# Kernel optimization log

Measured on AMD Instinct MI355X. Metric: run time of the kernel, lower is better.

Reference implementation:

```python
import jax, jax.numpy as jnp
import numpy as np

B, H, S, D = 2, 16, 2048, 64

def setup_inputs() -> dict:
    key = jax.random.key(0)
    kq, kk, kv = jax.random.split(key, 3)
    q = jax.random.normal(kq, (B, H, S, D), dtype=jnp.float32)
    k = jax.random.normal(kk, (B, H, S, D), dtype=jnp.float32)
    v = jax.random.normal(kv, (B, H, S, D), dtype=jnp.float32)
    # causal mask, broadcastable over batch and heads
    mask = jnp.tril(jnp.ones((S, S), dtype=bool))[None, None, :, :]
    return {"q": q, "k": k, "v": v, "mask": mask}

def reference(q, k, v, mask):
    d_k = q.shape[-1]
    # scores: [B, H, S, S]
    scores = jnp.einsum('bhqd,bhkd->bhqk', q, k) / (d_k ** 0.5)
    scores = jnp.where(mask, scores, -jnp.inf)
    probs = jax.nn.softmax(scores, axis=-1)  # numerically stable (max-subtracted)
    return jnp.einsum('bhqk,bhkd->bhqd', probs, v)
```

## Files before the change

### kernel.cpp

```cpp
#include <hip/hip_runtime.h>

#define S_LEN 2048
#define DHEAD 64
#define NBH   32
#define QTILE 64
#define KVTILE 64
#define NQ 32
#define LDK 72

typedef float          f32x4  __attribute__((ext_vector_type(4)));
typedef unsigned short u16x8  __attribute__((ext_vector_type(8)));
typedef unsigned int   u32x2  __attribute__((ext_vector_type(2)));
typedef unsigned int   u32x4  __attribute__((ext_vector_type(4)));
typedef __bf16         bf16x8 __attribute__((ext_vector_type(8)));

__device__ __forceinline__ unsigned int pack_bf16(float lo, float hi) {
  return __builtin_amdgcn_perm(__builtin_bit_cast(unsigned int, hi),
                               __builtin_bit_cast(unsigned int, lo),
                               0x07060302u);
}

#define KVSTRIDE 9216
#define VOFF 4608
#define PB0 18432

__global__ __launch_bounds__(256, 2)
void attn_fwd_kernel(const float* __restrict__ qg, const float* __restrict__ kg,
                     const float* __restrict__ vg, float* __restrict__ og)
{
  __shared__ unsigned short smem[23040];

  const int tid  = threadIdx.x;
  const int wid  = tid >> 6;
  const int lane = tid & 63;
  const int lr   = lane & 15;
  const int lg   = lane >> 4;

  const int bid  = blockIdx.x;
  const int pair = bid >> 5;
  const int bh   = bid & 31;

  const float* qp = qg + (size_t)bh * S_LEN * DHEAD;
  const float* kp = kg + (size_t)bh * S_LEN * DHEAD;
  const float* vp = vg + (size_t)bh * S_LEN * DHEAD;
  float*       op = og + (size_t)bh * S_LEN * DHEAD;

  const int krow = tid >> 4;
  const int kcol = (tid & 15) * 4;
  const int va   = (wid << 2) | (tid & 3);
  const int vm   = (tid >> 2) & 15;
  const int PB   = PB0 + wid * 1152;

  f32x4 kx[4], vx[4];

  auto load_tile = [&](int kv0) {
    #pragma unroll
    for (int it = 0; it < 4; ++it)
      kx[it] = *reinterpret_cast<const f32x4*>(
          kp + (size_t)(kv0 + it * 16 + krow) * DHEAD + kcol);
    #pragma unroll
    for (int j = 0; j < 4; ++j)
      vx[j] = *reinterpret_cast<const f32x4*>(
          vp + (size_t)(kv0 + 4 * va + j) * DHEAD + 4 * vm);
  };

  auto stage = [&](int buf) {
    const int kb = buf * KVSTRIDE;
    const int vb = VOFF + buf * KVSTRIDE;
    #pragma unroll
    for (int it = 0; it < 4; ++it) {
      u32x2 w;
      w[0] = pack_bf16(kx[it][0], kx[it][1]);
      w[1] = pack_bf16(kx[it][2], kx[it][3]);
      *reinterpret_cast<u32x2*>(&smem[kb + (it * 16 + krow) * LDK + kcol]) = w;
    }
    #pragma unroll
    for (int c = 0; c < 4; ++c) {
      u32x2 w;
      w[0] = pack_bf16(vx[0][c], vx[1][c]);
      w[1] = pack_bf16(vx[2][c], vx[3][c]);
      *reinterpret_cast<u32x2*>(&smem[vb + (4 * vm + c) * LDK + 4 * va]) = w;
    }
  };

  #pragma unroll 1
  for (int half = 0; half < 2; ++half) {
    const int qt  = half ? (NQ - 1 - pair) : pair;
    const int q0w = qt * QTILE + wid * 16;

    const float qscale = 0.125f * 1.44269504f;
    bf16x8 qf[2];
    #pragma unroll
    for (int f = 0; f < 2; ++f) {
      const f32x4* src = reinterpret_cast<const f32x4*>(
          qp + (size_t)(q0w + lr) * DHEAD + f * 32 + lg * 8);
      f32x4 x0 = src[0];
      f32x4 x1 = src[1];
      u32x4 qw;
      qw[0] = pack_bf16(x0[0] * qscale, x0[1] * qscale);
      qw[1] = pack_bf16(x0[2] * qscale, x0[3] * qscale);
      qw[2] = pack_bf16(x1[0] * qscale, x1[1] * qscale);
      qw[3] = pack_bf16(x1[2] * qscale, x1[3] * qscale);
      qf[f] = __builtin_bit_cast(bf16x8, qw);
    }

    f32x4 oacc[4] = {};
    float lsum = 0.f;

    load_tile(0);
    stage(0);
    __syncthreads();

    for (int t = 0; t <= qt; ++t) {
      const int cur = t & 1;
      const int kv0 = t * KVTILE;
      const bool pre = (t < qt);

      if (pre) load_tile(kv0 + KVTILE);

      f32x4 sacc[4] = {};
      const int kbase = cur * KVSTRIDE;
      __builtin_amdgcn_s_setprio(1);
      #pragma unroll
      for (int cb = 0; cb < 4; ++cb) {
        const int krd = kbase + (cb * 16 + lr) * LDK;
        #pragma unroll
        for (int f = 0; f < 2; ++f) {
          bf16x8 kb8 = __builtin_bit_cast(bf16x8,
              *reinterpret_cast<const u16x8*>(&smem[krd + f * 32 + lg * 8]));
          sacc[cb] = __builtin_amdgcn_mfma_f32_16x16x32_bf16(kb8, qf[f], sacc[cb], 0, 0, 0);
        }
      }
      __builtin_amdgcn_s_setprio(0);

      const bool diag = (t == qt);
      const int rowq = q0w + lr;
      #pragma unroll
      for (int cb = 0; cb < 4; ++cb) {
        float p[4];
        #pragma unroll
        for (int rr = 0; rr < 4; ++rr) {
          p[rr] = __builtin_amdgcn_exp2f(sacc[cb][rr]);
          if (diag && (kv0 + cb * 16 + lg * 4 + rr > rowq)) p[rr] = 0.f;
        }
        lsum += (p[0] + p[1]) + (p[2] + p[3]);
        u32x2 w;
        w[0] = pack_bf16(p[0], p[1]);
        w[1] = pack_bf16(p[2], p[3]);
        *reinterpret_cast<u32x2*>(&smem[PB + lr * LDK + cb * 16 + lg * 4]) = w;
      }

      bf16x8 pb8[2];
      #pragma unroll
      for (int ks = 0; ks < 2; ++ks)
        pb8[ks] = __builtin_bit_cast(bf16x8,
            *reinterpret_cast<const u16x8*>(&smem[PB + lr * LDK + ks * 32 + lg * 8]));
      const int vbase = VOFF + cur * KVSTRIDE;
      __builtin_amdgcn_s_setprio(1);
      #pragma unroll
      for (int db = 0; db < 4; ++db) {
        const int vrd = vbase + (db * 16 + lr) * LDK;
        #pragma unroll
        for (int ks = 0; ks < 2; ++ks) {
          bf16x8 va8 = __builtin_bit_cast(bf16x8,
              *reinterpret_cast<const u16x8*>(&smem[vrd + ks * 32 + lg * 8]));
          oacc[db] = __builtin_amdgcn_mfma_f32_16x16x32_bf16(va8, pb8[ks], oacc[db], 0, 0, 0);
        }
      }
      __builtin_amdgcn_s_setprio(0);

      if (pre) stage(cur ^ 1);

      __syncthreads();
    }

    lsum += __shfl_xor(lsum, 16, 64);
    lsum += __shfl_xor(lsum, 32, 64);
    const float rl = 1.0f / lsum;
    #pragma unroll
    for (int db = 0; db < 4; ++db) {
      f32x4 o;
      #pragma unroll
      for (int rr = 0; rr < 4; ++rr) o[rr] = oacc[db][rr] * rl;
      *reinterpret_cast<f32x4*>(
          op + (size_t)(q0w + lr) * DHEAD + db * 16 + lg * 4) = o;
    }
  }
}

extern "C" void kernel_launch(void* const* d_in, const int* in_sizes, int n_in,
                              void* d_out, int out_size, void* d_ws, size_t ws_size,
                              hipStream_t stream) {
  const float* q = (const float*)d_in[0];
  const float* k = (const float*)d_in[1];
  const float* v = (const float*)d_in[2];
  float* out = (float*)d_out;

  dim3 grid(16 * NBH);
  dim3 block(256);
  attn_fwd_kernel<<<grid, block, 0, stream>>>(q, k, v, out);
}
```

Measured before the change: 48.15 us.

## Use 512-thread blocks with 128-row Q tiles and split K/V loading roles

Each block now has 8 waves covering a 128-row query tile, so one staged K/V tile serves twice as many query rows. Blocks pair short and long causal tiles across the grid index. Loading is split so waves 0-3 fetch K and waves 4-7 fetch V, which halves per-thread prefetch registers. Waves whose diagonal comes earlier sit idle through later tiles but still take part in the barriers, and each wave writes its output at its diagonal step.

```diff
diff --git a/kernel.cpp b/kernel.cpp
--- a/kernel.cpp
+++ b/kernel.cpp
@@ -2,10 +2,7 @@
 
 #define S_LEN 2048
 #define DHEAD 64
-#define NBH   32
-#define QTILE 64
 #define KVTILE 64
-#define NQ 32
 #define LDK 72
 
 typedef float          f32x4  __attribute__((ext_vector_type(4)));
@@ -20,15 +17,15 @@
                                0x07060302u);
 }
 
+#define KVHALF 4608
 #define KVSTRIDE 9216
-#define VOFF 4608
 #define PB0 18432
 
-__global__ __launch_bounds__(256, 2)
+__global__ __launch_bounds__(512, 4)
 void attn_fwd_kernel(const float* __restrict__ qg, const float* __restrict__ kg,
                      const float* __restrict__ vg, float* __restrict__ og)
 {
-  __shared__ unsigned short smem[23040];
+  __shared__ unsigned short smem[27648];
 
   const int tid  = threadIdx.x;
   const int wid  = tid >> 6;
@@ -36,87 +33,98 @@
   const int lr   = lane & 15;
   const int lg   = lane >> 4;
 
-  const int bid  = blockIdx.x;
-  const int pair = bid >> 5;
-  const int bh   = bid & 31;
+  const int bid = blockIdx.x;
+  const int bh  = bid >> 4;
+  const int r   = bid & 15;
+  const int qt2 = (r < 8) ? r : 23 - r;
+
+  const int q0w  = qt2 * 128 + wid * 16;
+  const int tb   = q0w >> 6;
+  const int tmax = 2 * qt2 + 1;
 
   const float* qp = qg + (size_t)bh * S_LEN * DHEAD;
   const float* kp = kg + (size_t)bh * S_LEN * DHEAD;
   const float* vp = vg + (size_t)bh * S_LEN * DHEAD;
   float*       op = og + (size_t)bh * S_LEN * DHEAD;
 
-  const int krow = tid >> 4;
-  const int kcol = (tid & 15) * 4;
-  const int va   = (wid << 2) | (tid & 3);
-  const int vm   = (tid >> 2) & 15;
-  const int PB   = PB0 + wid * 1152;
-
-  f32x4 kx[4], vx[4];
+  const bool krole = (wid < 4);
+  const int  krow  = tid >> 4;
+  const int  kcol  = (tid & 15) * 4;
+  const int  vtid  = tid - 256;
+  const int  va    = ((vtid >> 6) << 2) | (vtid & 3);
+  const int  vm    = (vtid >> 2) & 15;
+
+  f32x4 rx[4];
 
   auto load_tile = [&](int kv0) {
-    #pragma unroll
-    for (int it = 0; it < 4; ++it)
-      kx[it] = *reinterpret_cast<const f32x4*>(
-          kp + (size_t)(kv0 + it * 16 + krow) * DHEAD + kcol);
-    #pragma unroll
-    for (int j = 0; j < 4; ++j)
-      vx[j] = *reinterpret_cast<const f32x4*>(
-          vp + (size_t)(kv0 + 4 * va + j) * DHEAD + 4 * vm);
-  };
-
-  auto stage = [&](int buf) {
-    const int kb = buf * KVSTRIDE;
-    const int vb = VOFF + buf * KVSTRIDE;
-    #pragma unroll
-    for (int it = 0; it < 4; ++it) {
-      u32x2 w;
-      w[0] = pack_bf16(kx[it][0], kx[it][1]);
-      w[1] = pack_bf16(kx[it][2], kx[it][3]);
-      *reinterpret_cast<u32x2*>(&smem[kb + (it * 16 + krow) * LDK + kcol]) = w;
-    }
-    #pragma unroll
-    for (int c = 0; c < 4; ++c) {
-      u32x2 w;
-      w[0] = pack_bf16(vx[0][c], vx[1][c]);
-      w[1] = pack_bf16(vx[2][c], vx[3][c]);
-      *reinterpret_cast<u32x2*>(&smem[vb + (4 * vm + c) * LDK + 4 * va]) = w;
+    if (krole) {
+      #pragma unroll
+      for (int it = 0; it < 4; ++it)
+        rx[it] = *reinterpret_cast<const f32x4*>(
+            kp + (size_t)(kv0 + it * 16 + krow) * DHEAD + kcol);
+    } else {
+      #pragma unroll
+      for (int j = 0; j < 4; ++j)
+        rx[j] = *reinterpret_cast<const f32x4*>(
+            vp + (size_t)(kv0 + 4 * va + j) * DHEAD + 4 * vm);
     }
   };
 
-  #pragma unroll 1
-  for (int half = 0; half < 2; ++half) {
-    const int qt  = half ? (NQ - 1 - pair) : pair;
-    const int q0w = qt * QTILE + wid * 16;
-
-    const float qscale = 0.125f * 1.44269504f;
-    bf16x8 qf[2];
-    #pragma unroll
-    for (int f = 0; f < 2; ++f) {
-      const f32x4* src = reinterpret_cast<const f32x4*>(
-          qp + (size_t)(q0w + lr) * DHEAD + f * 32 + lg * 8);
-      f32x4 x0 = src[0];
-      f32x4 x1 = src[1];
-      u32x4 qw;
-      qw[0] = pack_bf16(x0[0] * qscale, x0[1] * qscale);
-      qw[1] = pack_bf16(x0[2] * qscale, x0[3] * qscale);
-      qw[2] = pack_bf16(x1[0] * qscale, x1[1] * qscale);
-      qw[3] = pack_bf16(x1[2] * qscale, x1[3] * qscale);
-      qf[f] = __builtin_bit_cast(bf16x8, qw);
+  auto stage = [&](int buf) {
+    if (krole) {
+      const int kb = buf * KVSTRIDE;
+      #pragma unroll
+      for (int it = 0; it < 4; ++it) {
+        u32x2 w;
+        w[0] = pack_bf16(rx[it][0], rx[it][1]);
+        w[1] = pack_bf16(rx[it][2], rx[it][3]);
+        *reinterpret_cast<u32x2*>(&smem[kb + (it * 16 + krow) * LDK + kcol]) = w;
+      }
+    } else {
+      const int vb = KVHALF + buf * KVSTRIDE;
+      #pragma unroll
+      for (int c = 0; c < 4; ++c) {
+        u32x2 w;
+        w[0] = pack_bf16(rx[0][c], rx[1][c]);
+        w[1] = pack_bf16(rx[2][c], rx[3][c]);
+        *reinterpret_cast<u32x2*>(&smem[vb + (4 * vm + c) * LDK + 4 * va]) = w;
+      }
     }
-
-    f32x4 oacc[4] = {};
-    float lsum = 0.f;
-
-    load_tile(0);
-    stage(0);
-    __syncthreads();
-
-    for (int t = 0; t <= qt; ++t) {
-      const int cur = t & 1;
+  };
+
+  const float qscale = 0.125f * 1.44269504f;
+  bf16x8 qf[2];
+  #pragma unroll
+  for (int f = 0; f < 2; ++f) {
+    const f32x4* src = reinterpret_cast<const f32x4*>(
+        qp + (size_t)(q0w + lr) * DHEAD + f * 32 + lg * 8);
+    f32x4 x0 = src[0];
+    f32x4 x1 = src[1];
+    u32x4 qw;
+    qw[0] = pack_bf16(x0[0] * qscale, x0[1] * qscale);
+    qw[1] = pack_bf16(x0[2] * qscale, x0[3] * qscale);
+    qw[2] = pack_bf16(x1[0] * qscale, x1[1] * qscale);
+    qw[3] = pack_bf16(x1[2] * qscale, x1[3] * qscale);
+    qf[f] = __builtin_bit_cast(bf16x8, qw);
+  }
+
+  f32x4 oacc[4] = {};
+  float lsum = 0.f;
+
+  load_tile(0);
+  stage(0);
+  __syncthreads();
+
+  const int PB = PB0 + wid * 1152;
+
+  for (int t = 0; t <= tmax; ++t) {
+    const int cur = t & 1;
+    const bool pre = (t < tmax);
+
+    if (pre) load_tile((t + 1) * KVTILE);
+
+    if (t <= tb) {
       const int kv0 = t * KVTILE;
-      const bool pre = (t < qt);
-
-      if (pre) load_tile(kv0 + KVTILE);
 
       f32x4 sacc[4] = {};
       const int kbase = cur * KVSTRIDE;
@@ -133,15 +141,15 @@
       }
       __builtin_amdgcn_s_setprio(0);
 
-      const bool diag = (t == qt);
-      const int rowq = q0w + lr;
+      const bool diag = (t == tb);
+      const int limit = q0w + lr - kv0;
       #pragma unroll
       for (int cb = 0; cb < 4; ++cb) {
         float p[4];
         #pragma unroll
         for (int rr = 0; rr < 4; ++rr) {
           p[rr] = __builtin_amdgcn_exp2f(sacc[cb][rr]);
-          if (diag && (kv0 + cb * 16 + lg * 4 + rr > rowq)) p[rr] = 0.f;
+          if (diag && (cb * 16 + lg * 4 + rr > limit)) p[rr] = 0.f;
         }
         lsum += (p[0] + p[1]) + (p[2] + p[3]);
         u32x2 w;
@@ -155,7 +163,7 @@
       for (int ks = 0; ks < 2; ++ks)
         pb8[ks] = __builtin_bit_cast(bf16x8,
             *reinterpret_cast<const u16x8*>(&smem[PB + lr * LDK + ks * 32 + lg * 8]));
-      const int vbase = VOFF + cur * KVSTRIDE;
+      const int vbase = KVHALF + cur * KVSTRIDE;
       __builtin_amdgcn_s_setprio(1);
       #pragma unroll
       for (int db = 0; db < 4; ++db) {
@@ -169,22 +177,25 @@
       }
       __builtin_amdgcn_s_setprio(0);
 
-      if (pre) stage(cur ^ 1);
-
-      __syncthreads();
+      if (diag) {
+        float ls = lsum;
+        ls += __shfl_xor(ls, 16, 64);
+        ls += __shfl_xor(ls, 32, 64);
+        const float rl = 1.0f / ls;
+        #pragma unroll
+        for (int db = 0; db < 4; ++db) {
+          f32x4 o;
+          #pragma unroll
+          for (int rr = 0; rr < 4; ++rr) o[rr] = oacc[db][rr] * rl;
+          *reinterpret_cast<f32x4*>(
+              op + (size_t)(q0w + lr) * DHEAD + db * 16 + lg * 4) = o;
+        }
+      }
     }
 
-    lsum += __shfl_xor(lsum, 16, 64);
-    lsum += __shfl_xor(lsum, 32, 64);
-    const float rl = 1.0f / lsum;
-    #pragma unroll
-    for (int db = 0; db < 4; ++db) {
-      f32x4 o;
-      #pragma unroll
-      for (int rr = 0; rr < 4; ++rr) o[rr] = oacc[db][rr] * rl;
-      *reinterpret_cast<f32x4*>(
-          op + (size_t)(q0w + lr) * DHEAD + db * 16 + lg * 4) = o;
-    }
+    if (pre) stage(cur ^ 1);
+
+    __syncthreads();
   }
 }
 
@@ -196,7 +207,7 @@
   const float* v = (const float*)d_in[2];
   float* out = (float*)d_out;
 
-  dim3 grid(16 * NBH);
-  dim3 block(256);
+  dim3 grid(32 * 16);
+  dim3 block(512);
   attn_fwd_kernel<<<grid, block, 0, stream>>>(q, k, v, out);
 }
```

Measured after the change: 63.90 us. 1.33x slower.
